# Kernel tuning notes

Hardware: AMD Instinct MI355X
Metric: run time of the kernel (lower is better)

The kernel has to match this reference:

```python
import jax, jax.numpy as jnp
import numpy as np

NUM_VECTORS = 8192
LATENT_DIM = 256
BETA = 0.25
B, H, W = 16, 32, 32


def setup_inputs() -> dict:
    key = jax.random.key(0)
    k1, k2, k3 = jax.random.split(key, 3)
    x = jax.random.normal(k1, (B, LATENT_DIM, H, W), dtype=jnp.float32)
    # embedding_key.weight.data.uniform_(-1/num_vectors, 1/num_vectors)
    emb_key = jax.random.uniform(
        k2, (NUM_VECTORS, LATENT_DIM), dtype=jnp.float32,
        minval=-1.0 / NUM_VECTORS, maxval=1.0 / NUM_VECTORS)
    # orthogonal init for embedding_value
    a = np.asarray(jax.random.normal(k3, (LATENT_DIM, LATENT_DIM), dtype=jnp.float32))
    q, r = np.linalg.qr(a)
    q = q * np.sign(np.diag(r))  # make deterministic-ish orthogonal
    emb_value = jnp.asarray(q, dtype=jnp.float32)
    return {"x": x, "emb_key": emb_key, "emb_value": emb_value}


def reference(x, emb_key, emb_value):
    b, c, h, w = x.shape
    xt = jnp.transpose(x, (0, 2, 3, 1))          # b h w c
    xf = xt.reshape(-1, c)                       # (bhw) c
    d = (jnp.sum(xf * xf, axis=1, keepdims=True)
         + jnp.sum(emb_key * emb_key, axis=1)
         - 2.0 * (xf @ emb_key.T))               # (bhw) K
    idx = jnp.argmin(d, axis=1)                  # (bhw,)
    xq = emb_key[idx] @ emb_value                # (bhw) c
    xq = xq.reshape(xt.shape)                    # b h w c
    xq_grad = jnp.transpose(xq, (0, 3, 1, 2))    # b c h w
    sg = jax.lax.stop_gradient
    loss = jnp.mean((sg(xq) - xt) ** 2) + BETA * jnp.mean((xq - sg(xt)) ** 2)
    xq_st = xt + sg(xq - xt)                     # straight-through
    xq_st = jnp.transpose(xq_st, (0, 3, 1, 2))   # b c h w
    return xq_st, xq_grad, idx, loss
```

## Files before the change

### kernel.cpp

```cpp
#include <hip/hip_runtime.h>
#include <cfloat>

#define LATENT 256
#define NV 8192
#define NROWS 16384
#define HW 1024
#define CHW (LATENT * HW)
#define PLANE 4194304
#define IDX_OFF (2 * PLANE)
#define LOSS_OFF (IDX_OFF + NROWS)
#define MARGIN_S 6e-4f
#define CAP 2048

typedef __bf16 bf16x8 __attribute__((ext_vector_type(8)));
typedef float f32x4 __attribute__((ext_vector_type(4)));

typedef __attribute__((address_space(1))) const unsigned int GU32;
typedef __attribute__((address_space(3))) unsigned int SU32;
#define GLOAD16(gp, sp) __builtin_amdgcn_global_load_lds((GU32*)(gp), (SU32*)(sp), 16, 0, 0)

__device__ inline unsigned short f2bf(float f) {
  unsigned u = __builtin_bit_cast(unsigned, f);
  u = u + 0x7FFFu + ((u >> 16) & 1u);
  return (unsigned short)(u >> 16);
}
__device__ inline float bf2f(unsigned short h) {
  return __builtin_bit_cast(float, (unsigned)h << 16);
}

__global__ __launch_bounds__(256) void prep_ek(const float* __restrict__ ek,
                                               unsigned short* __restrict__ ek_hi) {
  int i = (blockIdx.x * 256 + threadIdx.x) << 3;
  float4 a = *(const float4*)(ek + i);
  float4 b = *(const float4*)(ek + i + 4);
  ushort4 h0, h1;
  h0.x = f2bf(a.x); h0.y = f2bf(a.y); h0.z = f2bf(a.z); h0.w = f2bf(a.w);
  h1.x = f2bf(b.x); h1.y = f2bf(b.y); h1.z = f2bf(b.z); h1.w = f2bf(b.w);
  *(ushort4*)(ek_hi + i) = h0;
  *(ushort4*)(ek_hi + i + 4) = h1;
}

__global__ __launch_bounds__(256) void prep_x(const float* __restrict__ x,
                                              unsigned short* __restrict__ x_hi) {
  __shared__ float tile[64][68];
  const int t = threadIdx.x;
  const int b = blockIdx.x >> 6;
  const int c0 = ((blockIdx.x >> 4) & 3) << 6;
  const int hw0 = (blockIdx.x & 15) << 6;
  #pragma unroll
  for (int p = 0; p < 4; ++p) {
    int id = (p << 8) + t;
    int r = id >> 4;
    int h4 = (id & 15) << 2;
    float4 v = *(const float4*)(x + (size_t)b * CHW + (size_t)(c0 + r) * HW + hw0 + h4);
    *(float4*)&tile[r][h4] = v;
  }
  __syncthreads();
  #pragma unroll
  for (int p = 0; p < 4; ++p) {
    int id = (p << 8) + t;
    int rh = id >> 4;
    int c4 = (id & 15) << 2;
    ushort4 h;
    h.x = f2bf(tile[c4][rh]);     h.y = f2bf(tile[c4 + 1][rh]);
    h.z = f2bf(tile[c4 + 2][rh]); h.w = f2bf(tile[c4 + 3][rh]);
    *(ushort4*)(x_hi + (size_t)((b << 10) + hw0 + rh) * LATENT + c0 + c4) = h;
  }
}

__global__ __launch_bounds__(256, 4) void phaseA(const unsigned short* __restrict__ ek_hi,
                                                 const unsigned short* __restrict__ x_hi,
                                                 unsigned* __restrict__ smax) {
  __shared__ unsigned short As[2][4][128][8];
  __shared__ unsigned short Bs[2][4][128][8];
  const int t = threadIdx.x;
  const int mt = blockIdx.x & 63;
  const int panel = blockIdx.x >> 6;
  const int m0 = mt << 7, r0 = panel << 7;
  const int sr = t & 127;
  const int sside = t >> 7;
  const unsigned short* src = sside ? x_hi + (size_t)(r0 + sr) * LATENT
                                    : ek_hi + (size_t)(m0 + sr) * LATENT;
  const int row0 = ((t >> 6) & 1) << 6;
  unsigned short (*SD)[4][128][8] = sside ? Bs : As;
#define STAGEA(buf, kc) { \
    const unsigned short* g_ = src + ((kc) << 5); \
    GLOAD16(g_,      &SD[buf][0][row0][0]); \
    GLOAD16(g_ + 8,  &SD[buf][1][row0][0]); \
    GLOAD16(g_ + 16, &SD[buf][2][row0][0]); \
    GLOAD16(g_ + 24, &SD[buf][3][row0][0]); }
  STAGEA(0, 0);
  const int w = t >> 6, l = t & 63;
  const int lm = l & 15, q4 = l >> 4;
  const int mw = (w & 1) << 6;
  const int nw = (w >> 1) << 6;
  f32x4 acc[4][4];
  #pragma unroll
  for (int ms = 0; ms < 4; ++ms)
    #pragma unroll
    for (int ns = 0; ns < 4; ++ns) acc[ms][ns] = (f32x4){0.f, 0.f, 0.f, 0.f};
  for (int kc = 0; kc < 8; ++kc) {
    const int buf = kc & 1;
    __syncthreads();
    if (kc < 7) STAGEA(buf ^ 1, kc + 1);
    bf16x8 a[4], b[4];
    #pragma unroll
    for (int ms = 0; ms < 4; ++ms)
      a[ms] = *(const bf16x8*)&As[buf][q4][mw + (ms << 4) + lm][0];
    #pragma unroll
    for (int ns = 0; ns < 4; ++ns)
      b[ns] = *(const bf16x8*)&Bs[buf][q4][nw + (ns << 4) + lm][0];
    #pragma unroll
    for (int ms = 0; ms < 4; ++ms)
      #pragma unroll
      for (int ns = 0; ns < 4; ++ns)
        acc[ms][ns] = __builtin_amdgcn_mfma_f32_16x16x32_bf16(a[ms], b[ns], acc[ms][ns], 0, 0, 0);
  }
  unsigned* stg = (unsigned*)&As[0][0][0][0];
  const int lbase = (l >> 4) << 2;
  #pragma unroll
  for (int ms = 0; ms < 4; ++ms) {
    #pragma unroll
    for (int ns = 0; ns < 4; ++ns) {
      f32x4 v4 = acc[ms][ns];
      float mx = fmaxf(fmaxf(v4[0], v4[1]), fmaxf(v4[2], v4[3]));
      mx = fmaxf(mx, __shfl_xor(mx, 16, 64));
      mx = fmaxf(mx, __shfl_xor(mx, 32, 64));
      float th = mx - MARGIN_S;
      unsigned mk = 0;
      #pragma unroll
      for (int r = 0; r < 4; ++r) if (v4[r] >= th) mk |= 1u << (lbase + r);
      mk |= (unsigned)__shfl_xor((int)mk, 16, 64);
      mk |= (unsigned)__shfl_xor((int)mk, 32, 64);
      if (l < 16) {
        int sloc = ((w & 1) << 2) + ms;
        int rloc = nw + (ns << 4) + l;
        stg[(sloc << 7) + rloc] = (unsigned)f2bf(mx) | (mk << 16);
      }
    }
  }
  __syncthreads();
  #pragma unroll
  for (int p = 0; p < 4; ++p) {
    int wid = (p << 8) + t;
    int sloc = wid >> 7;
    int rloc = wid & 127;
    smax[(size_t)((mt << 3) + sloc) * NROWS + r0 + rloc] = stg[wid];
  }
#undef STAGEA
}

__global__ __launch_bounds__(256) void phaseB(const float* __restrict__ x,
                                              const float* __restrict__ ek,
                                              const unsigned* __restrict__ smax,
                                              int* __restrict__ idxw,
                                              float* __restrict__ out) {
  __shared__ float xs[64][257];
  __shared__ float pmax[64][4];
  __shared__ float thrs[64];
  __shared__ float Xs[64];
  __shared__ unsigned long long best[64];
  __shared__ unsigned list[CAP];
  __shared__ int cnt;
  const int t = threadIdx.x;
  const int row0 = blockIdx.x << 6;
  const int b = row0 >> 10;
  const int hw0 = row0 & 1023;
  if (t == 0) cnt = 0;
  if (t < 64) best[t] = ~0ull;
  #pragma unroll
  for (int p = 0; p < 16; ++p) {
    int id = (p << 8) + t;
    int c = id >> 4;
    int r4 = (id & 15) << 2;
    float4 v = *(const float4*)(x + (size_t)b * CHW + (size_t)c * HW + hw0 + r4);
    xs[r4 + 0][c] = v.x; xs[r4 + 1][c] = v.y; xs[r4 + 2][c] = v.z; xs[r4 + 3][c] = v.w;
  }
  {
    const int r = t >> 2, q = t & 3;
    float m = -FLT_MAX;
    #pragma unroll 8
    for (int i = 0; i < 128; ++i) {
      unsigned wd = smax[(size_t)((i << 2) + q) * NROWS + row0 + r];
      m = fmaxf(m, bf2f((unsigned short)(wd & 0xffffu)));
    }
    pmax[r][q] = m;
  }
  __syncthreads();
  if (t < 64) {
    thrs[t] = fmaxf(fmaxf(pmax[t][0], pmax[t][1]), fmaxf(pmax[t][2], pmax[t][3])) - MARGIN_S;
    double s = 0.0;
    for (int c = 0; c < 256; ++c) {
      double v = (double)xs[t][c];
      s = fma(v, v, s);
    }
    Xs[t] = (float)s;
  }
  __syncthreads();
  {
    const int r = t >> 2, q = t & 3;
    const float thr = thrs[r];
    for (int i = 0; i < 128; ++i) {
      unsigned wd = smax[(size_t)((i << 2) + q) * NROWS + row0 + r];
      if (bf2f((unsigned short)(wd & 0xffffu)) >= thr) {
        unsigned mk = wd >> 16;
        int sidx = (i << 2) + q;
        while (mk) {
          int bit = __builtin_ctz(mk);
          mk &= mk - 1;
          int k = (sidx << 4) + bit;
          int slot = atomicAdd(&cnt, 1);
          if (slot < CAP) {
            list[slot] = ((unsigned)r << 13) | (unsigned)k;
          } else {
            const float* xr = &xs[r][0];
            const float* ep = ek + (size_t)k * LATENT;
            float f = 0.f;
            #pragma unroll 8
            for (int c = 0; c < 256; ++c) f = fmaf(xr[c], ep[c], f);
            float d = fmaf(-2.f, f, Xs[r]);
            unsigned u = __builtin_bit_cast(unsigned, d);
            u ^= (u >> 31) ? 0xFFFFFFFFu : 0x80000000u;
            atomicMin(&best[r], ((unsigned long long)u << 32) | (unsigned)k);
          }
        }
      }
    }
  }
  __syncthreads();
  const int n = cnt < CAP ? cnt : CAP;
  for (int i = t; i < n; i += 256) {
    unsigned enc = list[i];
    int r = enc >> 13;
    int k = enc & 0x1fff;
    const float* xr = &xs[r][0];
    const float* ep = ek + (size_t)k * LATENT;
    float f = 0.f;
    #pragma unroll 8
    for (int c = 0; c < 256; ++c) f = fmaf(xr[c], ep[c], f);
    float d = fmaf(-2.f, f, Xs[r]);
    unsigned u = __builtin_bit_cast(unsigned, d);
    u ^= (u >> 31) ? 0xFFFFFFFFu : 0x80000000u;
    atomicMin(&best[r], ((unsigned long long)u << 32) | (unsigned)k);
  }
  __syncthreads();
  if (t < 64) {
    int k = (int)(best[t] & 0xFFFFFFFFu);
    idxw[row0 + t] = k;
    out[IDX_OFF + row0 + t] = (float)k;
  }
}

__global__ __launch_bounds__(256) void out_kernel(
    const float* __restrict__ ek, const float* __restrict__ ev,
    const float* __restrict__ x, const int* __restrict__ idxw,
    float* __restrict__ out, float* __restrict__ bsum) {
  __shared__ float As[32][68];
  __shared__ float Vs[32][260];
  __shared__ int idx_s[64];
  __shared__ float red[256];
  const int t = threadIdx.x;
  const int blk = blockIdx.x;
  const int i0 = blk << 6;
  if (t < 64) idx_s[t] = idxw[i0 + t];
  const int ty = t >> 5;
  const int tx = t & 31;
  float acc[8][8];
  #pragma unroll
  for (int r = 0; r < 8; ++r)
    #pragma unroll
    for (int j = 0; j < 8; ++j) acc[r][j] = 0.f;
  for (int cc = 0; cc < 8; ++cc) {
    __syncthreads();
    {
      int r = t >> 2, cl = (t & 3) << 3;
      const float* eb = ek + (size_t)idx_s[r] * LATENT + (cc << 5) + cl;
      float4 v0 = *(const float4*)eb;
      float4 v1 = *(const float4*)(eb + 4);
      As[cl + 0][r] = v0.x; As[cl + 1][r] = v0.y;
      As[cl + 2][r] = v0.z; As[cl + 3][r] = v0.w;
      As[cl + 4][r] = v1.x; As[cl + 5][r] = v1.y;
      As[cl + 6][r] = v1.z; As[cl + 7][r] = v1.w;
    }
    {
      int c = t >> 3, jb = (t & 7) << 5;
      const float* vb = ev + (size_t)((cc << 5) + c) * LATENT + jb;
      float4* dst = (float4*)&Vs[c][jb];
      #pragma unroll
      for (int q = 0; q < 8; ++q) dst[q] = *(const float4*)(vb + 4 * q);
    }
    __syncthreads();
    #pragma unroll
    for (int c = 0; c < 32; ++c) {
      float a[8], bv[8];
      *(float4*)&a[0] = *(const float4*)&As[c][ty << 3];
      *(float4*)&a[4] = *(const float4*)&As[c][(ty << 3) + 4];
      *(float4*)&bv[0] = *(const float4*)&Vs[c][tx << 3];
      *(float4*)&bv[4] = *(const float4*)&Vs[c][(tx << 3) + 4];
      #pragma unroll
      for (int r = 0; r < 8; ++r)
        #pragma unroll
        for (int j = 0; j < 8; ++j) acc[r][j] = fmaf(a[r], bv[j], acc[r][j]);
    }
  }
  __syncthreads();
  const int bb = i0 >> 10;
  const int hwb = i0 & 1023;
  float* xL  = &As[0][0];
  float* stL = &Vs[0][0];
  float* xqL = stL + 32 * 68;
  const int ch = t >> 3;
  const int part = t & 7;
  float lsum = 0.f;
  for (int j = 0; j < 8; ++j) {
    {
      const float* xp = x + (size_t)bb * CHW + (size_t)((ch << 3) + j) * HW + hwb + (part << 3);
      *(float4*)&xL[ch * 68 + (part << 3)] = *(const float4*)xp;
      *(float4*)&xL[ch * 68 + (part << 3) + 4] = *(const float4*)(xp + 4);
    }
    __syncthreads();
    {
      #pragma unroll
      for (int r = 0; r < 8; ++r) {
        float xq = acc[r][j];
        float xt = xL[tx * 68 + (ty << 3) + r];
        float tmp = xq - xt;
        lsum = fmaf(tmp, tmp, lsum);
        stL[tx * 68 + (ty << 3) + r] = xt + tmp;
        xqL[tx * 68 + (ty << 3) + r] = xq;
      }
    }
    __syncthreads();
    {
      float* o0 = out + (size_t)bb * CHW + (size_t)((ch << 3) + j) * HW + hwb + (part << 3);
      float* o1 = o0 + PLANE;
      *(float4*)o0       = *(const float4*)&stL[ch * 68 + (part << 3)];
      *(float4*)(o0 + 4) = *(const float4*)&stL[ch * 68 + (part << 3) + 4];
      *(float4*)o1       = *(const float4*)&xqL[ch * 68 + (part << 3)];
      *(float4*)(o1 + 4) = *(const float4*)&xqL[ch * 68 + (part << 3) + 4];
    }
    __syncthreads();
  }
  red[t] = lsum;
  __syncthreads();
  for (int s = 128; s > 0; s >>= 1) {
    if (t < s) red[t] += red[t + s];
    __syncthreads();
  }
  if (t == 0) bsum[blk] = red[0];
}

__global__ __launch_bounds__(256) void fin_kernel(const float* __restrict__ bsum,
                                                  float* __restrict__ out) {
  __shared__ float red[256];
  int t = threadIdx.x;
  red[t] = bsum[t];
  __syncthreads();
  for (int s = 128; s > 0; s >>= 1) {
    if (t < s) red[t] += red[t + s];
    __syncthreads();
  }
  if (t == 0) {
    float m = red[0] / (float)PLANE;
    out[LOSS_OFF] = m + 0.25f * m;
  }
}

extern "C" void kernel_launch(void* const* d_in, const int* in_sizes, int n_in,
                              void* d_out, int out_size, void* d_ws, size_t ws_size,
                              hipStream_t stream) {
  const float* x = (const float*)d_in[0];
  const float* ek = (const float*)d_in[1];
  const float* ev = (const float*)d_in[2];
  float* out = (float*)d_out;
  char* base = (char*)d_ws;
  unsigned short* ek_hi = (unsigned short*)(base);
  unsigned short* x_hi  = (unsigned short*)(base + 4194304);
  int*            idxw  = (int*)(base + 12582912);
  float*          bsum  = (float*)(base + 12648448);
  unsigned* smax = (unsigned*)d_out;

  prep_ek<<<1024, 256, 0, stream>>>(ek, ek_hi);
  prep_x<<<1024, 256, 0, stream>>>(x, x_hi);
  phaseA<<<8192, 256, 0, stream>>>(ek_hi, x_hi, smax);
  phaseB<<<256, 256, 0, stream>>>(x, ek, smax, idxw, out);
  out_kernel<<<256, 256, 0, stream>>>(ek, ev, x, idxw, out, bsum);
  fin_kernel<<<1, 256, 0, stream>>>(bsum, out);
}
```

Baseline: 302.6 us.

## Enlarge phaseA tile to 128x256 with 512 threads and register-staged loads

The distance GEMM kernel now gives each block 128 codebook rows by 256 input rows, using 512 threads instead of 256, so it needs half as many blocks. Each codebook tile is loaded once per 256 input rows instead of once per 128, which cuts global and L2 traffic. The direct global-to-LDS load intrinsic is replaced by loads into registers followed by LDS stores placed after the MFMA loop, so the next chunk's fetch overlaps compute. This costs more registers and LDS per block, which may lower occupancy.

```diff
diff --git a/kernel.cpp b/kernel.cpp
--- a/kernel.cpp
+++ b/kernel.cpp
@@ -15,10 +15,6 @@
 typedef __bf16 bf16x8 __attribute__((ext_vector_type(8)));
 typedef float f32x4 __attribute__((ext_vector_type(4)));
 
-typedef __attribute__((address_space(1))) const unsigned int GU32;
-typedef __attribute__((address_space(3))) unsigned int SU32;
-#define GLOAD16(gp, sp) __builtin_amdgcn_global_load_lds((GU32*)(gp), (SU32*)(sp), 16, 0, 0)
-
 __device__ inline unsigned short f2bf(float f) {
   unsigned u = __builtin_bit_cast(unsigned, f);
   u = u + 0x7FFFu + ((u >> 16) & 1u);
@@ -68,28 +64,30 @@
   }
 }
 
-__global__ __launch_bounds__(256, 4) void phaseA(const unsigned short* __restrict__ ek_hi,
+__global__ __launch_bounds__(512, 6) void phaseA(const unsigned short* __restrict__ ek_hi,
                                                  const unsigned short* __restrict__ x_hi,
                                                  unsigned* __restrict__ smax) {
   __shared__ unsigned short As[2][4][128][8];
-  __shared__ unsigned short Bs[2][4][128][8];
+  __shared__ unsigned short Bs[2][4][256][8];
   const int t = threadIdx.x;
   const int mt = blockIdx.x & 63;
   const int panel = blockIdx.x >> 6;
-  const int m0 = mt << 7, r0 = panel << 7;
-  const int sr = t & 127;
-  const int sside = t >> 7;
-  const unsigned short* src = sside ? x_hi + (size_t)(r0 + sr) * LATENT
-                                    : ek_hi + (size_t)(m0 + sr) * LATENT;
-  const int row0 = ((t >> 6) & 1) << 6;
-  unsigned short (*SD)[4][128][8] = sside ? Bs : As;
-#define STAGEA(buf, kc) { \
-    const unsigned short* g_ = src + ((kc) << 5); \
-    GLOAD16(g_,      &SD[buf][0][row0][0]); \
-    GLOAD16(g_ + 8,  &SD[buf][1][row0][0]); \
-    GLOAD16(g_ + 16, &SD[buf][2][row0][0]); \
-    GLOAD16(g_ + 24, &SD[buf][3][row0][0]); }
-  STAGEA(0, 0);
+  const int m0 = mt << 7, r0 = panel << 8;
+  const bool doStage = t < 384;
+  const int sB = t >= 128;
+  const int srow = sB ? (t - 128) : t;
+  const unsigned short* src = sB ? x_hi + (size_t)(r0 + srow) * LATENT
+                                 : ek_hi + (size_t)(m0 + srow) * LATENT;
+  uint4 reg[4];
+  if (doStage) {
+    #pragma unroll
+    for (int q = 0; q < 4; ++q) reg[q] = *(const uint4*)(src + (q << 3));
+    if (sB) {
+      for (int q = 0; q < 4; ++q) *(uint4*)&Bs[0][q][srow][0] = reg[q];
+    } else {
+      for (int q = 0; q < 4; ++q) *(uint4*)&As[0][q][srow][0] = reg[q];
+    }
+  }
   const int w = t >> 6, l = t & 63;
   const int lm = l & 15, q4 = l >> 4;
   const int mw = (w & 1) << 6;
@@ -102,7 +100,11 @@
   for (int kc = 0; kc < 8; ++kc) {
     const int buf = kc & 1;
     __syncthreads();
-    if (kc < 7) STAGEA(buf ^ 1, kc + 1);
+    if (kc < 7 && doStage) {
+      #pragma unroll
+      for (int q = 0; q < 4; ++q)
+        reg[q] = *(const uint4*)(src + ((kc + 1) << 5) + (q << 3));
+    }
     bf16x8 a[4], b[4];
     #pragma unroll
     for (int ms = 0; ms < 4; ++ms)
@@ -115,6 +117,13 @@
       #pragma unroll
       for (int ns = 0; ns < 4; ++ns)
         acc[ms][ns] = __builtin_amdgcn_mfma_f32_16x16x32_bf16(a[ms], b[ns], acc[ms][ns], 0, 0, 0);
+    if (kc < 7 && doStage) {
+      if (sB) {
+        for (int q = 0; q < 4; ++q) *(uint4*)&Bs[buf ^ 1][q][srow][0] = reg[q];
+      } else {
+        for (int q = 0; q < 4; ++q) *(uint4*)&As[buf ^ 1][q][srow][0] = reg[q];
+      }
+    }
   }
   unsigned* stg = (unsigned*)&As[0][0][0][0];
   const int lbase = (l >> 4) << 2;
@@ -135,19 +144,18 @@
       if (l < 16) {
         int sloc = ((w & 1) << 2) + ms;
         int rloc = nw + (ns << 4) + l;
-        stg[(sloc << 7) + rloc] = (unsigned)f2bf(mx) | (mk << 16);
+        stg[(sloc << 8) + rloc] = (unsigned)f2bf(mx) | (mk << 16);
       }
     }
   }
   __syncthreads();
   #pragma unroll
   for (int p = 0; p < 4; ++p) {
-    int wid = (p << 8) + t;
-    int sloc = wid >> 7;
-    int rloc = wid & 127;
+    int wid = (p << 9) + t;
+    int sloc = wid >> 8;
+    int rloc = wid & 255;
     smax[(size_t)((mt << 3) + sloc) * NROWS + r0 + rloc] = stg[wid];
   }
-#undef STAGEA
 }
 
 __global__ __launch_bounds__(256) void phaseB(const float* __restrict__ x,
@@ -382,7 +390,7 @@
 
   prep_ek<<<1024, 256, 0, stream>>>(ek, ek_hi);
   prep_x<<<1024, 256, 0, stream>>>(x, x_hi);
-  phaseA<<<8192, 256, 0, stream>>>(ek_hi, x_hi, smax);
+  phaseA<<<4096, 512, 0, stream>>>(ek_hi, x_hi, smax);
   phaseB<<<256, 256, 0, stream>>>(x, ek, smax, idxw, out);
   out_kernel<<<256, 256, 0, stream>>>(ek, ev, x, idxw, out, bsum);
   fin_kernel<<<1, 256, 0, stream>>>(bsum, out);
```

After: 687.5 us. +127.2%, slower.

## Merge prep kernels, stage GEMM tiles via registers, halve phaseB rows per block

Applied to the files above, without the earlier changes.

Combines the ek and x bf16 conversion kernels into one launch with a branch on block index. In phaseA, replaces direct global-to-LDS async loads with register-staged loads that are issued before the MFMA block and written to the other LDS buffer after it. phaseB now handles 32 rows per block across 512 blocks, with 8 threads per row scanning the candidate maxima, which gives more parallelism on the 256-CU device. The register staging adds register pressure and extra LDS write instructions in exchange for overlapping global latency with compute.

```diff
diff --git a/kernel.cpp b/kernel.cpp
--- a/kernel.cpp
+++ b/kernel.cpp
@@ -15,10 +15,6 @@
 typedef __bf16 bf16x8 __attribute__((ext_vector_type(8)));
 typedef float f32x4 __attribute__((ext_vector_type(4)));
 
-typedef __attribute__((address_space(1))) const unsigned int GU32;
-typedef __attribute__((address_space(3))) unsigned int SU32;
-#define GLOAD16(gp, sp) __builtin_amdgcn_global_load_lds((GU32*)(gp), (SU32*)(sp), 16, 0, 0)
-
 __device__ inline unsigned short f2bf(float f) {
   unsigned u = __builtin_bit_cast(unsigned, f);
   u = u + 0x7FFFu + ((u >> 16) & 1u);
@@ -28,25 +24,27 @@
   return __builtin_bit_cast(float, (unsigned)h << 16);
 }
 
-__global__ __launch_bounds__(256) void prep_ek(const float* __restrict__ ek,
-                                               unsigned short* __restrict__ ek_hi) {
-  int i = (blockIdx.x * 256 + threadIdx.x) << 3;
-  float4 a = *(const float4*)(ek + i);
-  float4 b = *(const float4*)(ek + i + 4);
-  ushort4 h0, h1;
-  h0.x = f2bf(a.x); h0.y = f2bf(a.y); h0.z = f2bf(a.z); h0.w = f2bf(a.w);
-  h1.x = f2bf(b.x); h1.y = f2bf(b.y); h1.z = f2bf(b.z); h1.w = f2bf(b.w);
-  *(ushort4*)(ek_hi + i) = h0;
-  *(ushort4*)(ek_hi + i + 4) = h1;
-}
-
-__global__ __launch_bounds__(256) void prep_x(const float* __restrict__ x,
-                                              unsigned short* __restrict__ x_hi) {
+__global__ __launch_bounds__(256) void prep_kernel(const float* __restrict__ ek,
+                                                   const float* __restrict__ x,
+                                                   unsigned short* __restrict__ ek_hi,
+                                                   unsigned short* __restrict__ x_hi) {
   __shared__ float tile[64][68];
   const int t = threadIdx.x;
-  const int b = blockIdx.x >> 6;
-  const int c0 = ((blockIdx.x >> 4) & 3) << 6;
-  const int hw0 = (blockIdx.x & 15) << 6;
+  if (blockIdx.x < 1024) {
+    int i = ((int)blockIdx.x * 256 + t) << 3;
+    float4 a = *(const float4*)(ek + i);
+    float4 b = *(const float4*)(ek + i + 4);
+    ushort4 h0, h1;
+    h0.x = f2bf(a.x); h0.y = f2bf(a.y); h0.z = f2bf(a.z); h0.w = f2bf(a.w);
+    h1.x = f2bf(b.x); h1.y = f2bf(b.y); h1.z = f2bf(b.z); h1.w = f2bf(b.w);
+    *(ushort4*)(ek_hi + i) = h0;
+    *(ushort4*)(ek_hi + i + 4) = h1;
+    return;
+  }
+  const int bid = blockIdx.x - 1024;
+  const int b = bid >> 6;
+  const int c0 = ((bid >> 4) & 3) << 6;
+  const int hw0 = (bid & 15) << 6;
   #pragma unroll
   for (int p = 0; p < 4; ++p) {
     int id = (p << 8) + t;
@@ -77,19 +75,18 @@
   const int mt = blockIdx.x & 63;
   const int panel = blockIdx.x >> 6;
   const int m0 = mt << 7, r0 = panel << 7;
+  const int sside = t >> 7;
   const int sr = t & 127;
-  const int sside = t >> 7;
   const unsigned short* src = sside ? x_hi + (size_t)(r0 + sr) * LATENT
                                     : ek_hi + (size_t)(m0 + sr) * LATENT;
-  const int row0 = ((t >> 6) & 1) << 6;
-  unsigned short (*SD)[4][128][8] = sside ? Bs : As;
-#define STAGEA(buf, kc) { \
-    const unsigned short* g_ = src + ((kc) << 5); \
-    GLOAD16(g_,      &SD[buf][0][row0][0]); \
-    GLOAD16(g_ + 8,  &SD[buf][1][row0][0]); \
-    GLOAD16(g_ + 16, &SD[buf][2][row0][0]); \
-    GLOAD16(g_ + 24, &SD[buf][3][row0][0]); }
-  STAGEA(0, 0);
+  uint4 reg[4];
+  #pragma unroll
+  for (int q = 0; q < 4; ++q) reg[q] = *(const uint4*)(src + (q << 3));
+  {
+    unsigned short (*dst)[128][8] = sside ? Bs[0] : As[0];
+    #pragma unroll
+    for (int q = 0; q < 4; ++q) *(uint4*)&dst[q][sr][0] = reg[q];
+  }
   const int w = t >> 6, l = t & 63;
   const int lm = l & 15, q4 = l >> 4;
   const int mw = (w & 1) << 6;
@@ -102,7 +99,11 @@
   for (int kc = 0; kc < 8; ++kc) {
     const int buf = kc & 1;
     __syncthreads();
-    if (kc < 7) STAGEA(buf ^ 1, kc + 1);
+    if (kc < 7) {
+      #pragma unroll
+      for (int q = 0; q < 4; ++q)
+        reg[q] = *(const uint4*)(src + ((kc + 1) << 5) + (q << 3));
+    }
     bf16x8 a[4], b[4];
     #pragma unroll
     for (int ms = 0; ms < 4; ++ms)
@@ -115,6 +116,11 @@
       #pragma unroll
       for (int ns = 0; ns < 4; ++ns)
         acc[ms][ns] = __builtin_amdgcn_mfma_f32_16x16x32_bf16(a[ms], b[ns], acc[ms][ns], 0, 0, 0);
+    if (kc < 7) {
+      unsigned short (*dst)[128][8] = sside ? Bs[buf ^ 1] : As[buf ^ 1];
+      #pragma unroll
+      for (int q = 0; q < 4; ++q) *(uint4*)&dst[q][sr][0] = reg[q];
+    }
   }
   unsigned* stg = (unsigned*)&As[0][0][0][0];
   const int lbase = (l >> 4) << 2;
@@ -147,7 +153,6 @@
     int rloc = wid & 127;
     smax[(size_t)((mt << 3) + sloc) * NROWS + r0 + rloc] = stg[wid];
   }
-#undef STAGEA
 }
 
 __global__ __launch_bounds__(256) void phaseB(const float* __restrict__ x,
@@ -155,40 +160,43 @@
                                               const unsigned* __restrict__ smax,
                                               int* __restrict__ idxw,
                                               float* __restrict__ out) {
-  __shared__ float xs[64][257];
-  __shared__ float pmax[64][4];
-  __shared__ float thrs[64];
-  __shared__ float Xs[64];
-  __shared__ unsigned long long best[64];
+  __shared__ float xs[32][257];
+  __shared__ float pmax[32][8];
+  __shared__ float thrs[32];
+  __shared__ float Xs[32];
+  __shared__ unsigned long long best[32];
   __shared__ unsigned list[CAP];
   __shared__ int cnt;
   const int t = threadIdx.x;
-  const int row0 = blockIdx.x << 6;
+  const int row0 = blockIdx.x << 5;
   const int b = row0 >> 10;
   const int hw0 = row0 & 1023;
   if (t == 0) cnt = 0;
-  if (t < 64) best[t] = ~0ull;
-  #pragma unroll
-  for (int p = 0; p < 16; ++p) {
+  if (t < 32) best[t] = ~0ull;
+  #pragma unroll
+  for (int p = 0; p < 8; ++p) {
     int id = (p << 8) + t;
-    int c = id >> 4;
-    int r4 = (id & 15) << 2;
+    int c = id >> 3;
+    int r4 = (id & 7) << 2;
     float4 v = *(const float4*)(x + (size_t)b * CHW + (size_t)c * HW + hw0 + r4);
     xs[r4 + 0][c] = v.x; xs[r4 + 1][c] = v.y; xs[r4 + 2][c] = v.z; xs[r4 + 3][c] = v.w;
   }
   {
-    const int r = t >> 2, q = t & 3;
+    const int r = t >> 3, q = t & 7;
     float m = -FLT_MAX;
     #pragma unroll 8
-    for (int i = 0; i < 128; ++i) {
-      unsigned wd = smax[(size_t)((i << 2) + q) * NROWS + row0 + r];
+    for (int i = 0; i < 64; ++i) {
+      unsigned wd = smax[(size_t)((i << 3) + q) * NROWS + row0 + r];
       m = fmaxf(m, bf2f((unsigned short)(wd & 0xffffu)));
     }
     pmax[r][q] = m;
   }
   __syncthreads();
-  if (t < 64) {
-    thrs[t] = fmaxf(fmaxf(pmax[t][0], pmax[t][1]), fmaxf(pmax[t][2], pmax[t][3])) - MARGIN_S;
+  if (t < 32) {
+    float m = pmax[t][0];
+    #pragma unroll
+    for (int q = 1; q < 8; ++q) m = fmaxf(m, pmax[t][q]);
+    thrs[t] = m - MARGIN_S;
     double s = 0.0;
     for (int c = 0; c < 256; ++c) {
       double v = (double)xs[t][c];
@@ -198,13 +206,13 @@
   }
   __syncthreads();
   {
-    const int r = t >> 2, q = t & 3;
+    const int r = t >> 3, q = t & 7;
     const float thr = thrs[r];
-    for (int i = 0; i < 128; ++i) {
-      unsigned wd = smax[(size_t)((i << 2) + q) * NROWS + row0 + r];
+    for (int i = 0; i < 64; ++i) {
+      unsigned wd = smax[(size_t)((i << 3) + q) * NROWS + row0 + r];
       if (bf2f((unsigned short)(wd & 0xffffu)) >= thr) {
         unsigned mk = wd >> 16;
-        int sidx = (i << 2) + q;
+        int sidx = (i << 3) + q;
         while (mk) {
           int bit = __builtin_ctz(mk);
           mk &= mk - 1;
@@ -244,7 +252,7 @@
     atomicMin(&best[r], ((unsigned long long)u << 32) | (unsigned)k);
   }
   __syncthreads();
-  if (t < 64) {
+  if (t < 32) {
     int k = (int)(best[t] & 0xFFFFFFFFu);
     idxw[row0 + t] = k;
     out[IDX_OFF + row0 + t] = (float)k;
@@ -380,10 +388,9 @@
   float*          bsum  = (float*)(base + 12648448);
   unsigned* smax = (unsigned*)d_out;
 
-  prep_ek<<<1024, 256, 0, stream>>>(ek, ek_hi);
-  prep_x<<<1024, 256, 0, stream>>>(x, x_hi);
+  prep_kernel<<<2048, 256, 0, stream>>>(ek, x, ek_hi, x_hi);
   phaseA<<<8192, 256, 0, stream>>>(ek_hi, x_hi, smax);
-  phaseB<<<256, 256, 0, stream>>>(x, ek, smax, idxw, out);
+  phaseB<<<512, 256, 0, stream>>>(x, ek, smax, idxw, out);
   out_kernel<<<256, 256, 0, stream>>>(ek, ev, x, idxw, out, bsum);
   fin_kernel<<<1, 256, 0, stream>>>(bsum, out);
 }
```

Result: faster. 244.7 us (median of 3 runs) (-19.1%).
